# Optimization experiments

Measured on AMD Instinct MI355X. Metric: run time of the kernel, lower is better.

Reference implementation:

```python
import jax, jax.numpy as jnp
import numpy as np
import math

B, N_NODES, N_EDGES = 2, 20000, 320000
IN_DIM, MODEL_DIM, NUM_HEADS = 128, 128, 8
HEAD_DIM = MODEL_DIM // NUM_HEADS
EPS = 1e-5


def setup_inputs() -> dict:
    key = jax.random.key(0)
    ks = jax.random.split(key, 12)
    s = 0.02
    x = jax.random.normal(ks[0], (B, N_NODES, IN_DIM), dtype=jnp.float32)
    edge_index = jax.random.randint(ks[1], (2, N_EDGES), 0, N_NODES, dtype=jnp.int32)
    return {
        "x": x,
        "proj_w": jax.random.normal(ks[2], (IN_DIM, MODEL_DIM), jnp.float32) * s,
        "wq_w": jax.random.normal(ks[3], (MODEL_DIM, MODEL_DIM), jnp.float32) * s,
        "wq_b": jax.random.normal(ks[4], (MODEL_DIM,), jnp.float32) * s,
        "wk_w": jax.random.normal(ks[5], (MODEL_DIM, MODEL_DIM), jnp.float32) * s,
        "wk_b": jax.random.normal(ks[6], (MODEL_DIM,), jnp.float32) * s,
        "wv_w": jax.random.normal(ks[7], (MODEL_DIM, MODEL_DIM), jnp.float32) * s,
        "wv_b": jax.random.normal(ks[8], (MODEL_DIM,), jnp.float32) * s,
        "ln_g": jnp.ones((MODEL_DIM,), jnp.float32),
        "ln_b": jnp.zeros((MODEL_DIM,), jnp.float32),
        "edge_index": edge_index,
    }


def reference(x, proj_w, wq_w, wq_b, wk_w, wk_b, wv_w, wv_b, ln_g, ln_b, edge_index):
    src, dst = edge_index[0], edge_index[1]
    scale = 1.0 / math.sqrt(HEAD_DIM)

    h = x @ proj_w                      # [B, N, D]  (dropout = identity in eval)
    lifted = h[:, src, :]               # [B, E, D] edge gather
    Q = lifted @ wq_w + wq_b
    K = lifted @ wk_w + wk_b
    V = lifted @ wv_w + wv_b

    alpha = jnp.sum(Q * K, axis=-1) * scale  # [B, E]

    def seg_softmax(a):  # a: [E]
        m = jax.ops.segment_max(a, dst, num_segments=N_NODES)
        m = jnp.where(jnp.isfinite(m), m, 0.0)
        e = jnp.exp(a - m[dst])
        s = jax.ops.segment_sum(e, dst, num_segments=N_NODES)
        return e / s[dst]

    attn = jax.vmap(seg_softmax)(alpha)           # [B, E]
    weighted_V = V * attn[..., None]              # [B, E, D]

    seg_sum = lambda t: jax.ops.segment_sum(t, dst, num_segments=N_NODES)
    agg = jax.vmap(seg_sum)(weighted_V)           # [B, N, D]

    counts = jax.ops.segment_sum(jnp.ones((N_EDGES,), jnp.float32), dst,
                                 num_segments=N_NODES)
    skip = jax.vmap(seg_sum)(lifted) / jnp.maximum(counts, 1.0)[None, :, None]

    out = agg + skip
    mu = jnp.mean(out, axis=-1, keepdims=True)
    var = jnp.var(out, axis=-1, keepdims=True)
    return (out - mu) * jax.lax.rsqrt(var + EPS) * ln_g + ln_b
```

## Files before the change

### kernel.cpp

```cpp
#include <hip/hip_runtime.h>
#include <hip/hip_bf16.h>

#define NNODES 20000
#define NEDGES 320000
#define BATCH  2
#define D      128
#define EPSF   1e-5f
#define QTILE_M 64
#define XS_LD   136
#define MAXDEG 64

typedef __attribute__((ext_vector_type(8))) short bf16x8;
typedef __attribute__((ext_vector_type(4))) float f32x4;

static __device__ __forceinline__ unsigned short f2bf(float f) {
    __hip_bfloat16 h = __float2bfloat16(f);
    return *reinterpret_cast<unsigned short*>(&h);
}
static __device__ __forceinline__ float bfu(unsigned short u) {
    union { unsigned int i; float f; } cv;
    cv.i = ((unsigned int)u) << 16;
    return cv.f;
}

__global__ __launch_bounds__(256) void prep_kernel(
    const float* __restrict__ Wp, const float* __restrict__ Wq,
    const float* __restrict__ Wk, const float* __restrict__ Wv,
    unsigned short* __restrict__ WF,
    int* __restrict__ cursor)
{
    int bid = blockIdx.x;
    if (bid < 32) {
        int sg = bid * 256 + threadIdx.x;
        int mat = sg >> 11, rem = sg & 2047;
        int f = rem >> 6, l = rem & 63;
        int nt = f >> 2, ks = f & 3;
        int c = l & 15, g = l >> 4;
        const float* W = (mat == 0) ? Wp : (mat == 1) ? Wq : (mat == 2) ? Wk : Wv;
        int n = nt * 16 + c;
        #pragma unroll
        for (int i = 0; i < 8; ++i) {
            int k = ks * 32 + g * 8 + i;
            WF[(size_t)sg * 8 + i] = f2bf(W[k * 128 + n]);
        }
    } else {
        int idx = (bid - 32) * 256 + threadIdx.x;
        if (idx < NNODES) cursor[idx] = 0;
    }
}

__global__ __launch_bounds__(256) void scatter_pad_kernel(
    const int* __restrict__ src, const int* __restrict__ dst,
    int* __restrict__ cursor,
    int* __restrict__ srcs_pad)
{
    int e = blockIdx.x * 256 + threadIdx.x;
    if (e >= NEDGES) return;
    int d = dst[e], s = src[e];
    int slot = atomicAdd(&cursor[d], 1);
    if (slot < MAXDEG) srcs_pad[d * MAXDEG + slot] = s;
}


__global__ __launch_bounds__(256) void qkv_mfma_kernel(
    const float* __restrict__ x,
    const unsigned short* __restrict__ WF,
    const float* __restrict__ Bq, const float* __restrict__ Bk, const float* __restrict__ Bv,
    unsigned short* __restrict__ hhv,
    float* __restrict__ a_out)
{
    __shared__ unsigned short Wbuf[16384];
    __shared__ unsigned short Hs[QTILE_M][XS_LD];
    const int t = threadIdx.x;
    const long row0 = (long)blockIdx.x * QTILE_M;
    const int w = t >> 6, l = t & 63;
    const int g = l >> 4, c = l & 15;
    const int rw = w * 16;

    bf16x8 wreg[8];
    #define LOAD_W_REGS(MAT_OFF)                                        \
        _Pragma("unroll")                                               \
        for (int q = 0; q < 8; ++q)                                     \
            wreg[q] = *(const bf16x8*)(WF + (MAT_OFF) + (q * 256 + t) * 8);
    #define WRITE_W_LDS()                                               \
        _Pragma("unroll")                                               \
        for (int q = 0; q < 8; ++q)                                     \
            *(bf16x8*)&Wbuf[(q * 256 + t) * 8] = wreg[q];

    LOAD_W_REGS(0)

    bf16x8 ax[4];
    {
        const float* xr = x + (row0 + rw + c) * D;
        #pragma unroll
        for (int ks = 0; ks < 4; ++ks) {
            float4 u0 = *(const float4*)(xr + ks * 32 + g * 8);
            float4 u1 = *(const float4*)(xr + ks * 32 + g * 8 + 4);
            bf16x8 f;
            f[0] = (short)f2bf(u0.x); f[1] = (short)f2bf(u0.y);
            f[2] = (short)f2bf(u0.z); f[3] = (short)f2bf(u0.w);
            f[4] = (short)f2bf(u1.x); f[5] = (short)f2bf(u1.y);
            f[6] = (short)f2bf(u1.z); f[7] = (short)f2bf(u1.w);
            ax[ks] = f;
        }
    }

    WRITE_W_LDS();
    __syncthreads();
    LOAD_W_REGS(16384)

    f32x4 hacc[8];
    #pragma unroll
    for (int nt = 0; nt < 8; ++nt) hacc[nt] = f32x4{0.f, 0.f, 0.f, 0.f};
    #pragma unroll
    for (int nt = 0; nt < 8; ++nt)
        #pragma unroll
        for (int ks = 0; ks < 4; ++ks) {
            bf16x8 b = *(const bf16x8*)&Wbuf[((nt * 4 + ks) * 64 + l) * 8];
            hacc[nt] = __builtin_amdgcn_mfma_f32_16x16x32_bf16(ax[ks], b, hacc[nt], 0, 0, 0);
        }
    #pragma unroll
    for (int nt = 0; nt < 8; ++nt)
        #pragma unroll
        for (int i = 0; i < 4; ++i)
            Hs[rw + 4 * g + i][nt * 16 + c] = f2bf(hacc[nt][i]);
    __syncthreads();

    #pragma unroll
    for (int q = 0; q < 4; ++q) {
        int ch = t + q * 256;
        int r = ch >> 4, off = (ch & 15) << 3;
        *(bf16x8*)(hhv + (row0 + r) * 256 + off) = *(const bf16x8*)&Hs[r][off];
    }
    bf16x8 ah[4];
    #pragma unroll
    for (int ks = 0; ks < 4; ++ks)
        ah[ks] = *(const bf16x8*)&Hs[rw + c][ks * 32 + g * 8];

    WRITE_W_LDS();
    __syncthreads();
    LOAD_W_REGS(32768)

    f32x4 qacc[8];
    #pragma unroll
    for (int nt = 0; nt < 8; ++nt) qacc[nt] = f32x4{0.f, 0.f, 0.f, 0.f};
    #pragma unroll
    for (int nt = 0; nt < 8; ++nt)
        #pragma unroll
        for (int ks = 0; ks < 4; ++ks) {
            bf16x8 b = *(const bf16x8*)&Wbuf[((nt * 4 + ks) * 64 + l) * 8];
            qacc[nt] = __builtin_amdgcn_mfma_f32_16x16x32_bf16(ah[ks], b, qacc[nt], 0, 0, 0);
        }
    __syncthreads();

    WRITE_W_LDS();
    __syncthreads();
    LOAD_W_REGS(49152)

    f32x4 kacc[8];
    #pragma unroll
    for (int nt = 0; nt < 8; ++nt) kacc[nt] = f32x4{0.f, 0.f, 0.f, 0.f};
    #pragma unroll
    for (int nt = 0; nt < 8; ++nt)
        #pragma unroll
        for (int ks = 0; ks < 4; ++ks) {
            bf16x8 b = *(const bf16x8*)&Wbuf[((nt * 4 + ks) * 64 + l) * 8];
            kacc[nt] = __builtin_amdgcn_mfma_f32_16x16x32_bf16(ah[ks], b, kacc[nt], 0, 0, 0);
        }
    __syncthreads();

    WRITE_W_LDS();
    __syncthreads();

    {
        float p[4] = {0.f, 0.f, 0.f, 0.f};
        #pragma unroll
        for (int nt = 0; nt < 8; ++nt) {
            float bq = Bq[nt * 16 + c];
            float bk = Bk[nt * 16 + c];
            #pragma unroll
            for (int i = 0; i < 4; ++i)
                p[i] += (qacc[nt][i] + bq) * (kacc[nt][i] + bk);
        }
        #pragma unroll
        for (int off = 1; off < 16; off <<= 1)
            #pragma unroll
            for (int i = 0; i < 4; ++i) p[i] += __shfl_xor(p[i], off, 64);
        if (c == 0)
            #pragma unroll
            for (int i = 0; i < 4; ++i)
                a_out[row0 + rw + 4 * g + i] = p[i] * 0.25f;
    }

    f32x4 vacc[8];
    #pragma unroll
    for (int nt = 0; nt < 8; ++nt) vacc[nt] = f32x4{0.f, 0.f, 0.f, 0.f};
    #pragma unroll
    for (int nt = 0; nt < 8; ++nt)
        #pragma unroll
        for (int ks = 0; ks < 4; ++ks) {
            bf16x8 b = *(const bf16x8*)&Wbuf[((nt * 4 + ks) * 64 + l) * 8];
            vacc[nt] = __builtin_amdgcn_mfma_f32_16x16x32_bf16(ah[ks], b, vacc[nt], 0, 0, 0);
        }
    #pragma unroll
    for (int nt = 0; nt < 8; ++nt) {
        float bv = Bv[nt * 16 + c];
        #pragma unroll
        for (int i = 0; i < 4; ++i)
            Hs[rw + 4 * g + i][nt * 16 + c] = f2bf(vacc[nt][i] + bv);
    }
    __syncthreads();
    #pragma unroll
    for (int q = 0; q < 4; ++q) {
        int ch = t + q * 256;
        int r = ch >> 4, off = (ch & 15) << 3;
        *(bf16x8*)(hhv + (row0 + r) * 256 + 128 + off) = *(const bf16x8*)&Hs[r][off];
    }
    #undef LOAD_W_REGS
    #undef WRITE_W_LDS
}


__global__ __launch_bounds__(256) void agg_kernel(
    const unsigned short* __restrict__ hhv,
    const float* __restrict__ a,
    const int* __restrict__ deg_arr,
    const int* __restrict__ srcs_pad,
    const float* __restrict__ ln_g, const float* __restrict__ ln_b,
    float* __restrict__ out)
{
    const int t = threadIdx.x;
    const int w = t >> 6, l = t & 63;
    const int flat = blockIdx.x * 4 + w;
    const int n = flat % NNODES;
    const int b = flat / NNODES;
    const int bN = b * NNODES;
    const int deg = min(deg_arr[n], MAXDEG);
    const bool valid = l < deg;

    int   sr_l = valid ? srcs_pad[n * MAXDEG + l] : 0;
    float av_l = valid ? a[bN + sr_l] : -1e30f;

    float m = av_l;
    #pragma unroll
    for (int off = 32; off >= 1; off >>= 1) m = fmaxf(m, __shfl_xor(m, off, 64));
    float e_l = valid ? __expf(av_l - m) : 0.f;
    float s = e_l;
    #pragma unroll
    for (int off = 32; off >= 1; off >>= 1) s += __shfl_xor(s, off, 64);
    const float inv_s = (deg > 0) ? 1.f / s : 0.f;
    const float inv_d = 1.f / (float)max(deg, 1);
    const float w_l = e_l * inv_s;

    const int q4 = l >> 4;
    const int cq = l & 15;
    float acc[8] = {0,0,0,0,0,0,0,0};
    float sk [8] = {0,0,0,0,0,0,0,0};
    const long rowArr = (long)bN * 256 + (cq << 3);

    if (deg > 0) {
        const int iters = (deg + 3) >> 2;
        long of0; float wj0, sw0;
        {
            int sel = q4;
            bool ev = sel < deg;
            int selc = ev ? sel : 0;
            int srj = __shfl(sr_l, selc, 64);
            float wj = __shfl(w_l, selc, 64);
            wj0 = ev ? wj : 0.f;
            sw0 = ev ? 1.f : 0.f;
            of0 = rowArr + (long)srj * 256;
        }
        bf16x8 h0  = *(const bf16x8*)(hhv + of0);
        bf16x8 hv0 = *(const bf16x8*)(hhv + of0 + 128);
        for (int jj = 0; jj < iters - 1; ++jj) {
            long of1; float wj1, sw1;
            {
                int sel = ((jj + 1) << 2) + q4;
                bool ev = sel < deg;
                int selc = ev ? sel : 0;
                int srj = __shfl(sr_l, selc, 64);
                float wj = __shfl(w_l, selc, 64);
                wj1 = ev ? wj : 0.f;
                sw1 = ev ? 1.f : 0.f;
                of1 = rowArr + (long)srj * 256;
            }
            bf16x8 h1  = *(const bf16x8*)(hhv + of1);
            bf16x8 hv1 = *(const bf16x8*)(hhv + of1 + 128);
            #pragma unroll
            for (int i = 0; i < 8; ++i) {
                acc[i] += wj0 * bfu((unsigned short)hv0[i]);
                sk[i]  += sw0 * bfu((unsigned short)h0[i]);
            }
            h0 = h1; hv0 = hv1; wj0 = wj1; sw0 = sw1;
        }
        #pragma unroll
        for (int i = 0; i < 8; ++i) {
            acc[i] += wj0 * bfu((unsigned short)hv0[i]);
            sk[i]  += sw0 * bfu((unsigned short)h0[i]);
        }
    }

    #pragma unroll
    for (int i = 0; i < 8; ++i) {
        acc[i] += __shfl_xor(acc[i], 32, 64);
        sk[i]  += __shfl_xor(sk[i],  32, 64);
        acc[i] += __shfl_xor(acc[i], 16, 64);
        sk[i]  += __shfl_xor(sk[i],  16, 64);
    }
    float v[8];
    float sum = 0.f, sq = 0.f;
    #pragma unroll
    for (int i = 0; i < 8; ++i) {
        v[i] = acc[i] + sk[i] * inv_d;
        sum += v[i];
        sq  += v[i] * v[i];
    }
    #pragma unroll
    for (int off = 8; off >= 1; off >>= 1) {
        sum += __shfl_xor(sum, off, 64);
        sq  += __shfl_xor(sq,  off, 64);
    }
    float mu   = sum * (1.f / 128.f);
    float var  = sq * (1.f / 128.f) - mu * mu;
    float rstd = rsqrtf(var + EPSF);
    if (q4 == 0) {
        float4 g0 = *(const float4*)(ln_g + (cq << 3));
        float4 g1 = *(const float4*)(ln_g + (cq << 3) + 4);
        float4 b0 = *(const float4*)(ln_b + (cq << 3));
        float4 b1 = *(const float4*)(ln_b + (cq << 3) + 4);
        float4 o0, o1;
        o0.x = (v[0] - mu) * rstd * g0.x + b0.x;
        o0.y = (v[1] - mu) * rstd * g0.y + b0.y;
        o0.z = (v[2] - mu) * rstd * g0.z + b0.z;
        o0.w = (v[3] - mu) * rstd * g0.w + b0.w;
        o1.x = (v[4] - mu) * rstd * g1.x + b1.x;
        o1.y = (v[5] - mu) * rstd * g1.y + b1.y;
        o1.z = (v[6] - mu) * rstd * g1.z + b1.z;
        o1.w = (v[7] - mu) * rstd * g1.w + b1.w;
        float* op = out + (long)flat * D + (cq << 3);
        *(float4*)op = o0;
        *(float4*)(op + 4) = o1;
    }
}


extern "C" void kernel_launch(void* const* d_in, const int* in_sizes, int n_in,
                              void* d_out, int out_size, void* d_ws, size_t ws_size,
                              hipStream_t stream)
{
    const float* x    = (const float*)d_in[0];
    const float* Wp   = (const float*)d_in[1];
    const float* Wq   = (const float*)d_in[2];
    const float* Bq   = (const float*)d_in[3];
    const float* Wk   = (const float*)d_in[4];
    const float* Bk   = (const float*)d_in[5];
    const float* Wv   = (const float*)d_in[6];
    const float* Bv   = (const float*)d_in[7];
    const float* ln_g = (const float*)d_in[8];
    const float* ln_b = (const float*)d_in[9];
    const int*   ei   = (const int*)d_in[10];
    const int* esrc = ei;
    const int* edst = ei + NEDGES;
    float* out = (float*)d_out;

    char* p = (char*)d_ws;
    auto alloc = [&](size_t bytes) -> char* {
        char* r = p;
        p += (bytes + 255) & ~(size_t)255;
        return r;
    };
    unsigned short* hhv = (unsigned short*)alloc((size_t)BATCH * NNODES * 256 * 2);
    float* a        = (float*)alloc((size_t)BATCH * NNODES * 4);
    int* cursor     = (int*)alloc((size_t)NNODES * 4);
    int* srcs_pad   = (int*)alloc((size_t)NNODES * MAXDEG * 4);
    unsigned short* WF = (unsigned short*)alloc((size_t)4 * 128 * 128 * 2);

    prep_kernel<<<111, 256, 0, stream>>>(Wp, Wq, Wk, Wv, WF, cursor);
    scatter_pad_kernel<<<(NEDGES + 255) / 256, 256, 0, stream>>>(esrc, edst, cursor, srcs_pad);
    qkv_mfma_kernel<<<(BATCH * NNODES) / QTILE_M, 256, 0, stream>>>(
        x, WF, Bq, Bk, Bv, hhv, a);
    agg_kernel<<<(BATCH * NNODES) / 4, 256, 0, stream>>>(
        hhv, a, cursor, srcs_pad, ln_g, ln_b, out);
}
```

Baseline: 164.4 us.

## Double QKV tile rows per wave and split agg gather across half-rows

The QKV MFMA kernel now processes 128 rows per block (two 16-row fragments per wave), so each LDS weight fragment feeds two MFMAs, and the weight staging and block count are halved. Bounds checks handle the ragged last tile. K and V accumulators are now computed per column tile to limit register pressure. The aggregation kernel drops the software-pipelined 4-edges-per-iteration gather: each lane now loads one 16-byte chunk (h or v half) for 2 edges per iteration, then recombines the two halves with shuffles. This trades register pressure and loss of prefetch overlap for fewer, more uniform loads.

```diff
diff --git a/kernel.cpp b/kernel.cpp
--- a/kernel.cpp
+++ b/kernel.cpp
@@ -6,9 +6,10 @@
 #define BATCH  2
 #define D      128
 #define EPSF   1e-5f
-#define QTILE_M 64
-#define XS_LD   136
+#define QTM    128
+#define XS_LD  136
 #define MAXDEG 64
+#define NROWS  (BATCH * NNODES)
 
 typedef __attribute__((ext_vector_type(8))) short bf16x8;
 typedef __attribute__((ext_vector_type(4))) float f32x4;
@@ -70,12 +71,12 @@
     float* __restrict__ a_out)
 {
     __shared__ unsigned short Wbuf[16384];
-    __shared__ unsigned short Hs[QTILE_M][XS_LD];
+    __shared__ unsigned short Hs[QTM][XS_LD];
     const int t = threadIdx.x;
-    const long row0 = (long)blockIdx.x * QTILE_M;
+    const long row0 = (long)blockIdx.x * QTM;
     const int w = t >> 6, l = t & 63;
     const int g = l >> 4, c = l & 15;
-    const int rw = w * 16;
+    const int rw = w * 32;
 
     bf16x8 wreg[8];
     #define LOAD_W_REGS(MAT_OFF)                                        \
@@ -89,9 +90,12 @@
 
     LOAD_W_REGS(0)
 
-    bf16x8 ax[4];
-    {
-        const float* xr = x + (row0 + rw + c) * D;
+    bf16x8 ax[2][4];
+    #pragma unroll
+    for (int rf = 0; rf < 2; ++rf) {
+        long r = row0 + rw + rf * 16 + c;
+        if (r >= NROWS) r = NROWS - 1;
+        const float* xr = x + r * D;
         #pragma unroll
         for (int ks = 0; ks < 4; ++ks) {
             float4 u0 = *(const float4*)(xr + ks * 32 + g * 8);
@@ -101,7 +105,7 @@
             f[2] = (short)f2bf(u0.z); f[3] = (short)f2bf(u0.w);
             f[4] = (short)f2bf(u1.x); f[5] = (short)f2bf(u1.y);
             f[6] = (short)f2bf(u1.z); f[7] = (short)f2bf(u1.w);
-            ax[ks] = f;
+            ax[rf][ks] = f;
         }
     }
 
@@ -109,112 +113,131 @@
     __syncthreads();
     LOAD_W_REGS(16384)
 
-    f32x4 hacc[8];
-    #pragma unroll
-    for (int nt = 0; nt < 8; ++nt) hacc[nt] = f32x4{0.f, 0.f, 0.f, 0.f};
+    f32x4 hacc[2][8];
+    #pragma unroll
+    for (int rf = 0; rf < 2; ++rf)
+        #pragma unroll
+        for (int nt = 0; nt < 8; ++nt) hacc[rf][nt] = f32x4{0.f, 0.f, 0.f, 0.f};
     #pragma unroll
     for (int nt = 0; nt < 8; ++nt)
         #pragma unroll
         for (int ks = 0; ks < 4; ++ks) {
             bf16x8 b = *(const bf16x8*)&Wbuf[((nt * 4 + ks) * 64 + l) * 8];
-            hacc[nt] = __builtin_amdgcn_mfma_f32_16x16x32_bf16(ax[ks], b, hacc[nt], 0, 0, 0);
-        }
+            #pragma unroll
+            for (int rf = 0; rf < 2; ++rf)
+                hacc[rf][nt] = __builtin_amdgcn_mfma_f32_16x16x32_bf16(ax[rf][ks], b, hacc[rf][nt], 0, 0, 0);
+        }
+    #pragma unroll
+    for (int rf = 0; rf < 2; ++rf)
+        #pragma unroll
+        for (int nt = 0; nt < 8; ++nt)
+            #pragma unroll
+            for (int i = 0; i < 4; ++i)
+                Hs[rw + rf * 16 + 4 * g + i][nt * 16 + c] = f2bf(hacc[rf][nt][i]);
+    __syncthreads();
+
+    #pragma unroll
+    for (int q = 0; q < 8; ++q) {
+        int ch = q * 256 + t;
+        int r = ch >> 4, off = (ch & 15) << 3;
+        if (row0 + r < NROWS)
+            *(bf16x8*)(hhv + (row0 + r) * 256 + off) = *(const bf16x8*)&Hs[r][off];
+    }
+    bf16x8 ah[2][4];
+    #pragma unroll
+    for (int rf = 0; rf < 2; ++rf)
+        #pragma unroll
+        for (int ks = 0; ks < 4; ++ks)
+            ah[rf][ks] = *(const bf16x8*)&Hs[rw + rf * 16 + c][ks * 32 + g * 8];
+
+    WRITE_W_LDS();
+    __syncthreads();
+    LOAD_W_REGS(32768)
+
+    f32x4 qacc[2][8];
+    #pragma unroll
+    for (int rf = 0; rf < 2; ++rf)
+        #pragma unroll
+        for (int nt = 0; nt < 8; ++nt) qacc[rf][nt] = f32x4{0.f, 0.f, 0.f, 0.f};
     #pragma unroll
     for (int nt = 0; nt < 8; ++nt)
         #pragma unroll
-        for (int i = 0; i < 4; ++i)
-            Hs[rw + 4 * g + i][nt * 16 + c] = f2bf(hacc[nt][i]);
-    __syncthreads();
-
-    #pragma unroll
-    for (int q = 0; q < 4; ++q) {
-        int ch = t + q * 256;
+        for (int ks = 0; ks < 4; ++ks) {
+            bf16x8 b = *(const bf16x8*)&Wbuf[((nt * 4 + ks) * 64 + l) * 8];
+            #pragma unroll
+            for (int rf = 0; rf < 2; ++rf)
+                qacc[rf][nt] = __builtin_amdgcn_mfma_f32_16x16x32_bf16(ah[rf][ks], b, qacc[rf][nt], 0, 0, 0);
+        }
+    __syncthreads();
+
+    WRITE_W_LDS();
+    __syncthreads();
+    LOAD_W_REGS(49152)
+
+    float p[2][4] = {{0.f,0.f,0.f,0.f},{0.f,0.f,0.f,0.f}};
+    #pragma unroll
+    for (int nt = 0; nt < 8; ++nt) {
+        f32x4 kacc[2] = {f32x4{0.f,0.f,0.f,0.f}, f32x4{0.f,0.f,0.f,0.f}};
+        #pragma unroll
+        for (int ks = 0; ks < 4; ++ks) {
+            bf16x8 b = *(const bf16x8*)&Wbuf[((nt * 4 + ks) * 64 + l) * 8];
+            #pragma unroll
+            for (int rf = 0; rf < 2; ++rf)
+                kacc[rf] = __builtin_amdgcn_mfma_f32_16x16x32_bf16(ah[rf][ks], b, kacc[rf], 0, 0, 0);
+        }
+        float bq = Bq[nt * 16 + c];
+        float bk = Bk[nt * 16 + c];
+        #pragma unroll
+        for (int rf = 0; rf < 2; ++rf)
+            #pragma unroll
+            for (int i = 0; i < 4; ++i)
+                p[rf][i] += (qacc[rf][nt][i] + bq) * (kacc[rf][i] + bk);
+    }
+    #pragma unroll
+    for (int off = 1; off < 16; off <<= 1)
+        #pragma unroll
+        for (int rf = 0; rf < 2; ++rf)
+            #pragma unroll
+            for (int i = 0; i < 4; ++i)
+                p[rf][i] += __shfl_xor(p[rf][i], off, 64);
+    if (c == 0) {
+        #pragma unroll
+        for (int rf = 0; rf < 2; ++rf)
+            #pragma unroll
+            for (int i = 0; i < 4; ++i) {
+                long r = row0 + rw + rf * 16 + 4 * g + i;
+                if (r < NROWS) a_out[r] = p[rf][i] * 0.25f;
+            }
+    }
+    __syncthreads();
+
+    WRITE_W_LDS();
+    __syncthreads();
+
+    #pragma unroll
+    for (int nt = 0; nt < 8; ++nt) {
+        f32x4 vacc[2] = {f32x4{0.f,0.f,0.f,0.f}, f32x4{0.f,0.f,0.f,0.f}};
+        #pragma unroll
+        for (int ks = 0; ks < 4; ++ks) {
+            bf16x8 b = *(const bf16x8*)&Wbuf[((nt * 4 + ks) * 64 + l) * 8];
+            #pragma unroll
+            for (int rf = 0; rf < 2; ++rf)
+                vacc[rf] = __builtin_amdgcn_mfma_f32_16x16x32_bf16(ah[rf][ks], b, vacc[rf], 0, 0, 0);
+        }
+        float bv = Bv[nt * 16 + c];
+        #pragma unroll
+        for (int rf = 0; rf < 2; ++rf)
+            #pragma unroll
+            for (int i = 0; i < 4; ++i)
+                Hs[rw + rf * 16 + 4 * g + i][nt * 16 + c] = f2bf(vacc[rf][i] + bv);
+    }
+    __syncthreads();
+    #pragma unroll
+    for (int q = 0; q < 8; ++q) {
+        int ch = q * 256 + t;
         int r = ch >> 4, off = (ch & 15) << 3;
-        *(bf16x8*)(hhv + (row0 + r) * 256 + off) = *(const bf16x8*)&Hs[r][off];
-    }
-    bf16x8 ah[4];
-    #pragma unroll
-    for (int ks = 0; ks < 4; ++ks)
-        ah[ks] = *(const bf16x8*)&Hs[rw + c][ks * 32 + g * 8];
-
-    WRITE_W_LDS();
-    __syncthreads();
-    LOAD_W_REGS(32768)
-
-    f32x4 qacc[8];
-    #pragma unroll
-    for (int nt = 0; nt < 8; ++nt) qacc[nt] = f32x4{0.f, 0.f, 0.f, 0.f};
-    #pragma unroll
-    for (int nt = 0; nt < 8; ++nt)
-        #pragma unroll
-        for (int ks = 0; ks < 4; ++ks) {
-            bf16x8 b = *(const bf16x8*)&Wbuf[((nt * 4 + ks) * 64 + l) * 8];
-            qacc[nt] = __builtin_amdgcn_mfma_f32_16x16x32_bf16(ah[ks], b, qacc[nt], 0, 0, 0);
-        }
-    __syncthreads();
-
-    WRITE_W_LDS();
-    __syncthreads();
-    LOAD_W_REGS(49152)
-
-    f32x4 kacc[8];
-    #pragma unroll
-    for (int nt = 0; nt < 8; ++nt) kacc[nt] = f32x4{0.f, 0.f, 0.f, 0.f};
-    #pragma unroll
-    for (int nt = 0; nt < 8; ++nt)
-        #pragma unroll
-        for (int ks = 0; ks < 4; ++ks) {
-            bf16x8 b = *(const bf16x8*)&Wbuf[((nt * 4 + ks) * 64 + l) * 8];
-            kacc[nt] = __builtin_amdgcn_mfma_f32_16x16x32_bf16(ah[ks], b, kacc[nt], 0, 0, 0);
-        }
-    __syncthreads();
-
-    WRITE_W_LDS();
-    __syncthreads();
-
-    {
-        float p[4] = {0.f, 0.f, 0.f, 0.f};
-        #pragma unroll
-        for (int nt = 0; nt < 8; ++nt) {
-            float bq = Bq[nt * 16 + c];
-            float bk = Bk[nt * 16 + c];
-            #pragma unroll
-            for (int i = 0; i < 4; ++i)
-                p[i] += (qacc[nt][i] + bq) * (kacc[nt][i] + bk);
-        }
-        #pragma unroll
-        for (int off = 1; off < 16; off <<= 1)
-            #pragma unroll
-            for (int i = 0; i < 4; ++i) p[i] += __shfl_xor(p[i], off, 64);
-        if (c == 0)
-            #pragma unroll
-            for (int i = 0; i < 4; ++i)
-                a_out[row0 + rw + 4 * g + i] = p[i] * 0.25f;
-    }
-
-    f32x4 vacc[8];
-    #pragma unroll
-    for (int nt = 0; nt < 8; ++nt) vacc[nt] = f32x4{0.f, 0.f, 0.f, 0.f};
-    #pragma unroll
-    for (int nt = 0; nt < 8; ++nt)
-        #pragma unroll
-        for (int ks = 0; ks < 4; ++ks) {
-            bf16x8 b = *(const bf16x8*)&Wbuf[((nt * 4 + ks) * 64 + l) * 8];
-            vacc[nt] = __builtin_amdgcn_mfma_f32_16x16x32_bf16(ah[ks], b, vacc[nt], 0, 0, 0);
-        }
-    #pragma unroll
-    for (int nt = 0; nt < 8; ++nt) {
-        float bv = Bv[nt * 16 + c];
-        #pragma unroll
-        for (int i = 0; i < 4; ++i)
-            Hs[rw + 4 * g + i][nt * 16 + c] = f2bf(vacc[nt][i] + bv);
-    }
-    __syncthreads();
-    #pragma unroll
-    for (int q = 0; q < 4; ++q) {
-        int ch = t + q * 256;
-        int r = ch >> 4, off = (ch & 15) << 3;
-        *(bf16x8*)(hhv + (row0 + r) * 256 + 128 + off) = *(const bf16x8*)&Hs[r][off];
+        if (row0 + r < NROWS)
+            *(bf16x8*)(hhv + (row0 + r) * 256 + 128 + off) = *(const bf16x8*)&Hs[r][off];
     }
     #undef LOAD_W_REGS
     #undef WRITE_W_LDS
@@ -252,67 +275,43 @@
     const float inv_d = 1.f / (float)max(deg, 1);
     const float w_l = e_l * inv_s;
 
-    const int q4 = l >> 4;
-    const int cq = l & 15;
+    const int eh   = l >> 5;
+    const int half = (l >> 4) & 1;
+    const int cq   = l & 15;
     float acc[8] = {0,0,0,0,0,0,0,0};
-    float sk [8] = {0,0,0,0,0,0,0,0};
-    const long rowArr = (long)bN * 256 + (cq << 3);
-
-    if (deg > 0) {
-        const int iters = (deg + 3) >> 2;
-        long of0; float wj0, sw0;
-        {
-            int sel = q4;
-            bool ev = sel < deg;
-            int selc = ev ? sel : 0;
-            int srj = __shfl(sr_l, selc, 64);
-            float wj = __shfl(w_l, selc, 64);
-            wj0 = ev ? wj : 0.f;
-            sw0 = ev ? 1.f : 0.f;
-            of0 = rowArr + (long)srj * 256;
-        }
-        bf16x8 h0  = *(const bf16x8*)(hhv + of0);
-        bf16x8 hv0 = *(const bf16x8*)(hhv + of0 + 128);
-        for (int jj = 0; jj < iters - 1; ++jj) {
-            long of1; float wj1, sw1;
-            {
-                int sel = ((jj + 1) << 2) + q4;
-                bool ev = sel < deg;
-                int selc = ev ? sel : 0;
-                int srj = __shfl(sr_l, selc, 64);
-                float wj = __shfl(w_l, selc, 64);
-                wj1 = ev ? wj : 0.f;
-                sw1 = ev ? 1.f : 0.f;
-                of1 = rowArr + (long)srj * 256;
-            }
-            bf16x8 h1  = *(const bf16x8*)(hhv + of1);
-            bf16x8 hv1 = *(const bf16x8*)(hhv + of1 + 128);
-            #pragma unroll
-            for (int i = 0; i < 8; ++i) {
-                acc[i] += wj0 * bfu((unsigned short)hv0[i]);
-                sk[i]  += sw0 * bfu((unsigned short)h0[i]);
-            }
-            h0 = h1; hv0 = hv1; wj0 = wj1; sw0 = sw1;
-        }
-        #pragma unroll
-        for (int i = 0; i < 8; ++i) {
-            acc[i] += wj0 * bfu((unsigned short)hv0[i]);
-            sk[i]  += sw0 * bfu((unsigned short)h0[i]);
-        }
-    }
-
+    const long rowBase = (long)bN * 256 + half * 128 + (cq << 3);
+
+    const int iters = (deg + 1) >> 1;
+    for (int jj = 0; jj < iters; ++jj) {
+        int sel = (jj << 1) + eh;
+        bool ev = sel < deg;
+        int selc = ev ? sel : 0;
+        int srj  = __shfl(sr_l, selc, 64);
+        float wj = __shfl(w_l,  selc, 64);
+        float mul = half ? (ev ? wj : 0.f) : (ev ? 1.f : 0.f);
+        bf16x8 d = *(const bf16x8*)(hhv + rowBase + (long)srj * 256);
+        #pragma unroll
+        for (int i = 0; i < 8; ++i)
+            acc[i] += mul * bfu((unsigned short)d[i]);
+    }
+
+    float accv[8], sk[8];
     #pragma unroll
     for (int i = 0; i < 8; ++i) {
-        acc[i] += __shfl_xor(acc[i], 32, 64);
-        sk[i]  += __shfl_xor(sk[i],  32, 64);
-        acc[i] += __shfl_xor(acc[i], 16, 64);
-        sk[i]  += __shfl_xor(sk[i],  16, 64);
+        float other = __shfl_xor(acc[i], 16, 64);
+        accv[i] = half ? acc[i] : other;
+        sk[i]   = half ? other  : acc[i];
+    }
+    #pragma unroll
+    for (int i = 0; i < 8; ++i) {
+        accv[i] += __shfl_xor(accv[i], 32, 64);
+        sk[i]   += __shfl_xor(sk[i],   32, 64);
     }
     float v[8];
     float sum = 0.f, sq = 0.f;
     #pragma unroll
     for (int i = 0; i < 8; ++i) {
-        v[i] = acc[i] + sk[i] * inv_d;
+        v[i] = accv[i] + sk[i] * inv_d;
         sum += v[i];
         sq  += v[i] * v[i];
     }
@@ -324,7 +323,7 @@
     float mu   = sum * (1.f / 128.f);
     float var  = sq * (1.f / 128.f) - mu * mu;
     float rstd = rsqrtf(var + EPSF);
-    if (q4 == 0) {
+    if (l < 16) {
         float4 g0 = *(const float4*)(ln_g + (cq << 3));
         float4 g1 = *(const float4*)(ln_g + (cq << 3) + 4);
         float4 b0 = *(const float4*)(ln_b + (cq << 3));
@@ -370,16 +369,16 @@
         p += (bytes + 255) & ~(size_t)255;
         return r;
     };
-    unsigned short* hhv = (unsigned short*)alloc((size_t)BATCH * NNODES * 256 * 2);
-    float* a        = (float*)alloc((size_t)BATCH * NNODES * 4);
+    unsigned short* hhv = (unsigned short*)alloc((size_t)NROWS * 256 * 2);
+    float* a        = (float*)alloc((size_t)NROWS * 4);
     int* cursor     = (int*)alloc((size_t)NNODES * 4);
     int* srcs_pad   = (int*)alloc((size_t)NNODES * MAXDEG * 4);
     unsigned short* WF = (unsigned short*)alloc((size_t)4 * 128 * 128 * 2);
 
     prep_kernel<<<111, 256, 0, stream>>>(Wp, Wq, Wk, Wv, WF, cursor);
     scatter_pad_kernel<<<(NEDGES + 255) / 256, 256, 0, stream>>>(esrc, edst, cursor, srcs_pad);
-    qkv_mfma_kernel<<<(BATCH * NNODES) / QTILE_M, 256, 0, stream>>>(
+    qkv_mfma_kernel<<<(NROWS + QTM - 1) / QTM, 256, 0, stream>>>(
         x, WF, Bq, Bk, Bv, hhv, a);
-    agg_kernel<<<(BATCH * NNODES) / 4, 256, 0, stream>>>(
+    agg_kernel<<<NROWS / 4, 256, 0, stream>>>(
         hhv, a, cursor, srcs_pad, ln_g, ln_b, out);
 }
```

New measurement: 168.6 us. 1.03x slower.

## Split fused QKV kernel into H/V and alpha kernels, restructure aggregation gather

Applied to the files above, without the earlier changes.

Splits the single projection kernel into one that computes H and V and one that reloads H to compute Q·K scores. This cuts live accumulator registers (K and V accumulators become per-tile rather than arrays) and uses per-wave LDS staging, which removes block-wide barriers. The aggregation kernel now splits each row fetch into H and V halves across half-waves and unrolls four edges per iteration for more loads in flight. The cost is an extra kernel launch and a re-read of H from global memory.

```diff
diff --git a/kernel.cpp b/kernel.cpp
--- a/kernel.cpp
+++ b/kernel.cpp
@@ -6,9 +6,10 @@
 #define BATCH  2
 #define D      128
 #define EPSF   1e-5f
-#define QTILE_M 64
-#define XS_LD   136
+#define QTM    64
+#define XS_LD  136
 #define MAXDEG 64
+#define NROWS  (BATCH * NNODES)
 
 typedef __attribute__((ext_vector_type(8))) short bf16x8;
 typedef __attribute__((ext_vector_type(4))) float f32x4;
@@ -61,31 +62,32 @@
     if (slot < MAXDEG) srcs_pad[d * MAXDEG + slot] = s;
 }
 
-
-__global__ __launch_bounds__(256) void qkv_mfma_kernel(
+#define DECL_STAGE_MACROS                                               \
+    bf16x8 wreg[8];
+#define LOAD_W_REGS(MAT_OFF)                                            \
+    _Pragma("unroll")                                                   \
+    for (int q = 0; q < 8; ++q)                                         \
+        wreg[q] = *(const bf16x8*)(WF + (MAT_OFF) + (q * 256 + t) * 8);
+#define WRITE_W_LDS()                                                   \
+    _Pragma("unroll")                                                   \
+    for (int q = 0; q < 8; ++q)                                         \
+        *(bf16x8*)&Wbuf[(q * 256 + t) * 8] = wreg[q];
+
+
+__global__ __launch_bounds__(256) void hv_kernel(
     const float* __restrict__ x,
     const unsigned short* __restrict__ WF,
-    const float* __restrict__ Bq, const float* __restrict__ Bk, const float* __restrict__ Bv,
-    unsigned short* __restrict__ hhv,
-    float* __restrict__ a_out)
+    const float* __restrict__ Bv,
+    unsigned short* __restrict__ hhv)
 {
     __shared__ unsigned short Wbuf[16384];
-    __shared__ unsigned short Hs[QTILE_M][XS_LD];
+    __shared__ unsigned short Hs[4][16][XS_LD];
     const int t = threadIdx.x;
-    const long row0 = (long)blockIdx.x * QTILE_M;
+    const long row0 = (long)blockIdx.x * QTM;
     const int w = t >> 6, l = t & 63;
     const int g = l >> 4, c = l & 15;
     const int rw = w * 16;
-
-    bf16x8 wreg[8];
-    #define LOAD_W_REGS(MAT_OFF)                                        \
-        _Pragma("unroll")                                               \
-        for (int q = 0; q < 8; ++q)                                     \
-            wreg[q] = *(const bf16x8*)(WF + (MAT_OFF) + (q * 256 + t) * 8);
-    #define WRITE_W_LDS()                                               \
-        _Pragma("unroll")                                               \
-        for (int q = 0; q < 8; ++q)                                     \
-            *(bf16x8*)&Wbuf[(q * 256 + t) * 8] = wreg[q];
+    DECL_STAGE_MACROS
 
     LOAD_W_REGS(0)
 
@@ -107,7 +109,7 @@
 
     WRITE_W_LDS();
     __syncthreads();
-    LOAD_W_REGS(16384)
+    LOAD_W_REGS(49152)
 
     f32x4 hacc[8];
     #pragma unroll
@@ -123,19 +125,67 @@
     for (int nt = 0; nt < 8; ++nt)
         #pragma unroll
         for (int i = 0; i < 4; ++i)
-            Hs[rw + 4 * g + i][nt * 16 + c] = f2bf(hacc[nt][i]);
-    __syncthreads();
+            Hs[w][4 * g + i][nt * 16 + c] = f2bf(hacc[nt][i]);
 
     #pragma unroll
     for (int q = 0; q < 4; ++q) {
-        int ch = t + q * 256;
+        int ch = q * 64 + l;
         int r = ch >> 4, off = (ch & 15) << 3;
-        *(bf16x8*)(hhv + (row0 + r) * 256 + off) = *(const bf16x8*)&Hs[r][off];
+        *(bf16x8*)(hhv + (row0 + rw + r) * 256 + off) = *(const bf16x8*)&Hs[w][r][off];
     }
     bf16x8 ah[4];
     #pragma unroll
     for (int ks = 0; ks < 4; ++ks)
-        ah[ks] = *(const bf16x8*)&Hs[rw + c][ks * 32 + g * 8];
+        ah[ks] = *(const bf16x8*)&Hs[w][c][ks * 32 + g * 8];
+
+    __syncthreads();
+    WRITE_W_LDS();
+    __syncthreads();
+
+    #pragma unroll
+    for (int nt = 0; nt < 8; ++nt) {
+        f32x4 vacc = f32x4{0.f, 0.f, 0.f, 0.f};
+        #pragma unroll
+        for (int ks = 0; ks < 4; ++ks) {
+            bf16x8 b = *(const bf16x8*)&Wbuf[((nt * 4 + ks) * 64 + l) * 8];
+            vacc = __builtin_amdgcn_mfma_f32_16x16x32_bf16(ah[ks], b, vacc, 0, 0, 0);
+        }
+        float bv = Bv[nt * 16 + c];
+        #pragma unroll
+        for (int i = 0; i < 4; ++i)
+            Hs[w][4 * g + i][nt * 16 + c] = f2bf(vacc[i] + bv);
+    }
+    #pragma unroll
+    for (int q = 0; q < 4; ++q) {
+        int ch = q * 64 + l;
+        int r = ch >> 4, off = (ch & 15) << 3;
+        *(bf16x8*)(hhv + (row0 + rw + r) * 256 + 128 + off) = *(const bf16x8*)&Hs[w][r][off];
+    }
+}
+
+__global__ __launch_bounds__(256) void alpha_kernel(
+    const unsigned short* __restrict__ hhv,
+    const unsigned short* __restrict__ WF,
+    const float* __restrict__ Bq, const float* __restrict__ Bk,
+    float* __restrict__ a_out)
+{
+    __shared__ unsigned short Wbuf[16384];
+    const int t = threadIdx.x;
+    const long row0 = (long)blockIdx.x * QTM;
+    const int w = t >> 6, l = t & 63;
+    const int g = l >> 4, c = l & 15;
+    const int rw = w * 16;
+    DECL_STAGE_MACROS
+
+    LOAD_W_REGS(16384)
+
+    bf16x8 ah[4];
+    {
+        const unsigned short* hr = hhv + (row0 + rw + c) * 256;
+        #pragma unroll
+        for (int ks = 0; ks < 4; ++ks)
+            ah[ks] = *(const bf16x8*)(hr + ks * 32 + g * 8);
+    }
 
     WRITE_W_LDS();
     __syncthreads();
@@ -152,74 +202,33 @@
             qacc[nt] = __builtin_amdgcn_mfma_f32_16x16x32_bf16(ah[ks], b, qacc[nt], 0, 0, 0);
         }
     __syncthreads();
-
     WRITE_W_LDS();
     __syncthreads();
-    LOAD_W_REGS(49152)
-
-    f32x4 kacc[8];
-    #pragma unroll
-    for (int nt = 0; nt < 8; ++nt) kacc[nt] = f32x4{0.f, 0.f, 0.f, 0.f};
-    #pragma unroll
-    for (int nt = 0; nt < 8; ++nt)
+
+    float p[4] = {0.f, 0.f, 0.f, 0.f};
+    #pragma unroll
+    for (int nt = 0; nt < 8; ++nt) {
+        f32x4 kacc = f32x4{0.f, 0.f, 0.f, 0.f};
         #pragma unroll
         for (int ks = 0; ks < 4; ++ks) {
             bf16x8 b = *(const bf16x8*)&Wbuf[((nt * 4 + ks) * 64 + l) * 8];
-            kacc[nt] = __builtin_amdgcn_mfma_f32_16x16x32_bf16(ah[ks], b, kacc[nt], 0, 0, 0);
-        }
-    __syncthreads();
-
-    WRITE_W_LDS();
-    __syncthreads();
-
-    {
-        float p[4] = {0.f, 0.f, 0.f, 0.f};
-        #pragma unroll
-        for (int nt = 0; nt < 8; ++nt) {
-            float bq = Bq[nt * 16 + c];
-            float bk = Bk[nt * 16 + c];
-            #pragma unroll
-            for (int i = 0; i < 4; ++i)
-                p[i] += (qacc[nt][i] + bq) * (kacc[nt][i] + bk);
-        }
-        #pragma unroll
-        for (int off = 1; off < 16; off <<= 1)
-            #pragma unroll
-            for (int i = 0; i < 4; ++i) p[i] += __shfl_xor(p[i], off, 64);
-        if (c == 0)
-            #pragma unroll
-            for (int i = 0; i < 4; ++i)
-                a_out[row0 + rw + 4 * g + i] = p[i] * 0.25f;
-    }
-
-    f32x4 vacc[8];
-    #pragma unroll
-    for (int nt = 0; nt < 8; ++nt) vacc[nt] = f32x4{0.f, 0.f, 0.f, 0.f};
-    #pragma unroll
-    for (int nt = 0; nt < 8; ++nt)
-        #pragma unroll
-        for (int ks = 0; ks < 4; ++ks) {
-            bf16x8 b = *(const bf16x8*)&Wbuf[((nt * 4 + ks) * 64 + l) * 8];
-            vacc[nt] = __builtin_amdgcn_mfma_f32_16x16x32_bf16(ah[ks], b, vacc[nt], 0, 0, 0);
-        }
-    #pragma unroll
-    for (int nt = 0; nt < 8; ++nt) {
-        float bv = Bv[nt * 16 + c];
+            kacc = __builtin_amdgcn_mfma_f32_16x16x32_bf16(ah[ks], b, kacc, 0, 0, 0);
+        }
+        float bq = Bq[nt * 16 + c];
+        float bk = Bk[nt * 16 + c];
         #pragma unroll
         for (int i = 0; i < 4; ++i)
-            Hs[rw + 4 * g + i][nt * 16 + c] = f2bf(vacc[nt][i] + bv);
-    }
-    __syncthreads();
-    #pragma unroll
-    for (int q = 0; q < 4; ++q) {
-        int ch = t + q * 256;
-        int r = ch >> 4, off = (ch & 15) << 3;
-        *(bf16x8*)(hhv + (row0 + r) * 256 + 128 + off) = *(const bf16x8*)&Hs[r][off];
-    }
-    #undef LOAD_W_REGS
-    #undef WRITE_W_LDS
-}
-
+            p[i] += (qacc[nt][i] + bq) * (kacc[i] + bk);
+    }
+    #pragma unroll
+    for (int off = 1; off < 16; off <<= 1)
+        #pragma unroll
+        for (int i = 0; i < 4; ++i) p[i] += __shfl_xor(p[i], off, 64);
+    if (c == 0)
+        #pragma unroll
+        for (int i = 0; i < 4; ++i)
+            a_out[row0 + rw + 4 * g + i] = p[i] * 0.25f;
+}
 
 __global__ __launch_bounds__(256) void agg_kernel(
     const unsigned short* __restrict__ hhv,
@@ -252,67 +261,60 @@
     const float inv_d = 1.f / (float)max(deg, 1);
     const float w_l = e_l * inv_s;
 
-    const int q4 = l >> 4;
-    const int cq = l & 15;
+    const int eh   = l >> 5;
+    const int half = (l >> 4) & 1;
+    const int cq   = l & 15;
     float acc[8] = {0,0,0,0,0,0,0,0};
-    float sk [8] = {0,0,0,0,0,0,0,0};
-    const long rowArr = (long)bN * 256 + (cq << 3);
-
-    if (deg > 0) {
-        const int iters = (deg + 3) >> 2;
-        long of0; float wj0, sw0;
-        {
-            int sel = q4;
-            bool ev = sel < deg;
-            int selc = ev ? sel : 0;
-            int srj = __shfl(sr_l, selc, 64);
-            float wj = __shfl(w_l, selc, 64);
-            wj0 = ev ? wj : 0.f;
-            sw0 = ev ? 1.f : 0.f;
-            of0 = rowArr + (long)srj * 256;
-        }
-        bf16x8 h0  = *(const bf16x8*)(hhv + of0);
-        bf16x8 hv0 = *(const bf16x8*)(hhv + of0 + 128);
-        for (int jj = 0; jj < iters - 1; ++jj) {
-            long of1; float wj1, sw1;
-            {
-                int sel = ((jj + 1) << 2) + q4;
-                bool ev = sel < deg;
-                int selc = ev ? sel : 0;
-                int srj = __shfl(sr_l, selc, 64);
-                float wj = __shfl(w_l, selc, 64);
-                wj1 = ev ? wj : 0.f;
-                sw1 = ev ? 1.f : 0.f;
-                of1 = rowArr + (long)srj * 256;
-            }
-            bf16x8 h1  = *(const bf16x8*)(hhv + of1);
-            bf16x8 hv1 = *(const bf16x8*)(hhv + of1 + 128);
-            #pragma unroll
-            for (int i = 0; i < 8; ++i) {
-                acc[i] += wj0 * bfu((unsigned short)hv0[i]);
-                sk[i]  += sw0 * bfu((unsigned short)h0[i]);
-            }
-            h0 = h1; hv0 = hv1; wj0 = wj1; sw0 = sw1;
-        }
-        #pragma unroll
-        for (int i = 0; i < 8; ++i) {
-            acc[i] += wj0 * bfu((unsigned short)hv0[i]);
-            sk[i]  += sw0 * bfu((unsigned short)h0[i]);
-        }
-    }
-
+    const long rowBase = (long)bN * 256 + half * 128 + (cq << 3);
+
+    #define PREP(JJ, OF, MU)  {                                         \
+        int sel = ((JJ) << 1) + eh;                                     \
+        bool ev = sel < deg;                                            \
+        int sc = ev ? sel : 0;                                          \
+        int srj = __shfl(sr_l, sc, 64);                                 \
+        float wj = __shfl(w_l, sc, 64);                                 \
+        MU = half ? (ev ? wj : 0.f) : (ev ? 1.f : 0.f);                 \
+        OF = rowBase + (long)srj * 256;  }
+
+    const int iters = (deg + 1) >> 1;
+    for (int j0 = 0; j0 < iters; j0 += 4) {
+        long oa, ob, oc, od; float ma, mb, mc, md;
+        PREP(j0,     oa, ma)
+        PREP(j0 + 1, ob, mb)
+        PREP(j0 + 2, oc, mc)
+        PREP(j0 + 3, od, md)
+        bf16x8 da = *(const bf16x8*)(hhv + oa);
+        bf16x8 db = *(const bf16x8*)(hhv + ob);
+        bf16x8 dc = *(const bf16x8*)(hhv + oc);
+        bf16x8 dd = *(const bf16x8*)(hhv + od);
+        #pragma unroll
+        for (int i = 0; i < 8; ++i) acc[i] += ma * bfu((unsigned short)da[i]);
+        #pragma unroll
+        for (int i = 0; i < 8; ++i) acc[i] += mb * bfu((unsigned short)db[i]);
+        #pragma unroll
+        for (int i = 0; i < 8; ++i) acc[i] += mc * bfu((unsigned short)dc[i]);
+        #pragma unroll
+        for (int i = 0; i < 8; ++i) acc[i] += md * bfu((unsigned short)dd[i]);
+    }
+    #undef PREP
+
+    float accv[8], sk[8];
     #pragma unroll
     for (int i = 0; i < 8; ++i) {
-        acc[i] += __shfl_xor(acc[i], 32, 64);
-        sk[i]  += __shfl_xor(sk[i],  32, 64);
-        acc[i] += __shfl_xor(acc[i], 16, 64);
-        sk[i]  += __shfl_xor(sk[i],  16, 64);
+        float other = __shfl_xor(acc[i], 16, 64);
+        accv[i] = half ? acc[i] : other;
+        sk[i]   = half ? other  : acc[i];
+    }
+    #pragma unroll
+    for (int i = 0; i < 8; ++i) {
+        accv[i] += __shfl_xor(accv[i], 32, 64);
+        sk[i]   += __shfl_xor(sk[i],   32, 64);
     }
     float v[8];
     float sum = 0.f, sq = 0.f;
     #pragma unroll
     for (int i = 0; i < 8; ++i) {
-        v[i] = acc[i] + sk[i] * inv_d;
+        v[i] = accv[i] + sk[i] * inv_d;
         sum += v[i];
         sq  += v[i] * v[i];
     }
@@ -324,7 +326,7 @@
     float mu   = sum * (1.f / 128.f);
     float var  = sq * (1.f / 128.f) - mu * mu;
     float rstd = rsqrtf(var + EPSF);
-    if (q4 == 0) {
+    if (l < 16) {
         float4 g0 = *(const float4*)(ln_g + (cq << 3));
         float4 g1 = *(const float4*)(ln_g + (cq << 3) + 4);
         float4 b0 = *(const float4*)(ln_b + (cq << 3));
@@ -370,16 +372,15 @@
         p += (bytes + 255) & ~(size_t)255;
         return r;
     };
-    unsigned short* hhv = (unsigned short*)alloc((size_t)BATCH * NNODES * 256 * 2);
-    float* a        = (float*)alloc((size_t)BATCH * NNODES * 4);
+    unsigned short* hhv = (unsigned short*)alloc((size_t)NROWS * 256 * 2);
+    float* a        = (float*)alloc((size_t)NROWS * 4);
     int* cursor     = (int*)alloc((size_t)NNODES * 4);
     int* srcs_pad   = (int*)alloc((size_t)NNODES * MAXDEG * 4);
     unsigned short* WF = (unsigned short*)alloc((size_t)4 * 128 * 128 * 2);
 
     prep_kernel<<<111, 256, 0, stream>>>(Wp, Wq, Wk, Wv, WF, cursor);
     scatter_pad_kernel<<<(NEDGES + 255) / 256, 256, 0, stream>>>(esrc, edst, cursor, srcs_pad);
-    qkv_mfma_kernel<<<(BATCH * NNODES) / QTILE_M, 256, 0, stream>>>(
-        x, WF, Bq, Bk, Bv, hhv, a);
-    agg_kernel<<<(BATCH * NNODES) / 4, 256, 0, stream>>>(
-        hhv, a, cursor, srcs_pad, ln_g, ln_b, out);
-}
+    hv_kernel<<<NROWS / QTM, 256, 0, stream>>>(x, WF, Bv, hhv);
+    alpha_kernel<<<NROWS / QTM, 256, 0, stream>>>(hhv, WF, Bq, Bk, a);
+    agg_kernel<<<NROWS / 4, 256, 0, stream>>>(hhv, a, cursor, srcs_pad, ln_g, ln_b, out);
+}
```

Result: no change. 164.3 us (-0.1%).
